# Optimization experiments

Hardware: AMD Instinct MI355X
Metric: run time of the kernel (lower is better)

The kernel has to match this reference:

```python
import jax, jax.numpy as jnp
import numpy as np
from jax import lax


def ternarize(w):
    """Standard TWN ternarization with straight-through estimator.
    delta = 0.7*mean(|w|); alpha = mean(|w|) over kept entries; w_t = alpha*sign(w)*mask.
    """
    a = jnp.abs(w)
    delta = 0.7 * a.mean()
    mask = (a > delta).astype(w.dtype)
    alpha = (a * mask).sum() / jnp.maximum(mask.sum(), 1.0)
    wt = alpha * jnp.sign(w) * mask
    return w + lax.stop_gradient(wt - w)  # STE


def conv3x3(x, w, b):
    y = lax.conv_general_dilated(x, ternarize(w), window_strides=(1, 1),
                                 padding=((1, 1), (1, 1)),
                                 dimension_numbers=('NCHW', 'OIHW', 'NCHW'))
    return y + b[None, :, None, None]


def maxpool2(x):
    return lax.reduce_window(x, -jnp.inf, lax.max, (1, 1, 2, 2), (1, 1, 2, 2), 'VALID')


def setup_inputs() -> dict:
    key = jax.random.key(0)
    ks = jax.random.split(key, 11)
    s = lambda k, shape, scale: jax.random.normal(k, shape, dtype=jnp.float32) * scale
    return {
        'x':   s(ks[0], (1024, 3, 32, 32), 1.0),
        'w1':  s(ks[1], (64, 3, 3, 3), 0.1),
        'b1':  s(ks[2], (64,), 0.01),
        'w2':  s(ks[3], (128, 64, 3, 3), 0.05),
        'b2':  s(ks[4], (128,), 0.01),
        'w3':  s(ks[5], (256, 128, 3, 3), 0.03),
        'b3':  s(ks[6], (256,), 0.01),
        'wf1': s(ks[7], (256, 4096), 0.02),
        'bf1': s(ks[8], (256,), 0.01),
        'wf2': s(ks[9], (10, 256), 0.06),
        'bf2': s(ks[10], (10,), 0.01),
    }


def reference(x, w1, b1, w2, b2, w3, b3, wf1, bf1, wf2, bf2):
    x = maxpool2(jax.nn.relu(conv3x3(x, w1, b1)))   # [B,64,16,16]
    x = maxpool2(jax.nn.relu(conv3x3(x, w2, b2)))   # [B,128,8,8]
    x = maxpool2(jax.nn.relu(conv3x3(x, w3, b3)))   # [B,256,4,4]
    x = x.reshape(-1, 256 * 4 * 4)
    x = jax.nn.relu(x @ ternarize(wf1).T + bf1)     # [B,256]
    return x @ ternarize(wf2).T + bf2               # [B,10]
```

## Files before the change

kernel.cpp:

```cpp
#include <hip/hip_runtime.h>
#include <hip/hip_bf16.h>


typedef __attribute__((ext_vector_type(8))) short short8;
typedef __attribute__((ext_vector_type(4))) float f32x4;
typedef __attribute__((ext_vector_type(4))) int i32x4;

#define GLOAD_LDS16(g, l)                                              \
    __builtin_amdgcn_global_load_lds(                                  \
        (const __attribute__((address_space(1))) void*)(g),            \
        (__attribute__((address_space(3))) void*)(l), 16, 0, 0)

__device__ __forceinline__ unsigned short f2bf(float x) {
    unsigned u = __float_as_uint(x);
    return (unsigned short)((u + 0x7fffu + ((u >> 16) & 1u)) >> 16);
}
__device__ __forceinline__ float bf2f(unsigned short b) {
    return __uint_as_float(((unsigned)b) << 16);
}

__device__ __forceinline__ float calc_S1(const double* __restrict__ scr,
                                         float amaxx) {
    const double c2 = scr[2];
    const float alpha1 = (float)(scr[1] / (c2 > 1.0 ? c2 : 1.0));
    const float ub = alpha1 * (float)scr[22] * amaxx + (float)scr[23];
    return 32512.0f / fmaxf(ub, 1e-30f);
}

#define WS_W1B   0
#define N_W1B    2048
#define WS_W2P   (WS_W1B + N_W1B)
#define N_W2P    (9*128*64)
#define WS_W3P   (WS_W2P + N_W2P)
#define N_W3P    (9*256*128)
#define WS_WTF1  (WS_W3P + N_W3P)
#define N_WTF1   (256*4096)
#define WS_WTF2  (WS_WTF1 + N_WTF1)
#define N_WTF2   (10*256)
#define WS_A1    (WS_WTF2 + N_WTF2)
#define N_A1     (1024*256*64)
#define WS_A2    (WS_A1 + N_A1)
#define N_A2     (1024*64*128)
#define WS_A3    (WS_A2 + N_A2)
#define N_A3     (1024*16*256)
#define WS_F1    (WS_A3 + N_A3)
#define N_F1     (1024*256)
#define WS_SCR   (WS_F1 + N_F1)

#define FC1_S    32

struct TernArgs {
    const float* w[6];
    int n[6];
};

__global__ void tern_stats1(TernArgs ta, double* __restrict__ scr) {
    const int wi = blockIdx.y;
    const float* __restrict__ w = ta.w[wi];
    const int n = ta.n[wi];
    __shared__ double red[4];
    const int lane = threadIdx.x & 63, wv = threadIdx.x >> 6;
    if (wi == 5) {
        float m = 0.f;
        for (int i = blockIdx.x * blockDim.x + threadIdx.x; i < n;
             i += gridDim.x * blockDim.x)
            m = fmaxf(m, fabsf(w[i]));
        #pragma unroll
        for (int off = 32; off > 0; off >>= 1)
            m = fmaxf(m, __shfl_down(m, off, 64));
        if (lane == 0) red[wv] = (double)m;
        __syncthreads();
        if (threadIdx.x == 0) {
            float mm = (float)fmax(fmax(red[0], red[1]), fmax(red[2], red[3]));
            atomicMax((int*)(scr + 20), __float_as_int(mm));
        }
        return;
    }
    double s = 0.0;
    for (int i = blockIdx.x * blockDim.x + threadIdx.x; i < n;
         i += gridDim.x * blockDim.x)
        s += (double)fabsf(w[i]);
    #pragma unroll
    for (int off = 32; off > 0; off >>= 1) s += __shfl_down(s, off, 64);
    if (lane == 0) red[wv] = s;
    __syncthreads();
    if (threadIdx.x == 0)
        atomicAdd(scr + wi * 4, red[0] + red[1] + red[2] + red[3]);
}

__global__ void tern_stats2(TernArgs ta, double* __restrict__ scr) {
    const int wi = blockIdx.y;
    const float* __restrict__ w = ta.w[wi];
    const int n = ta.n[wi];
    const float delta = (float)(0.7 * scr[wi * 4] / (double)n);
    double ms = 0.0, cnt = 0.0;
    for (int i = blockIdx.x * blockDim.x + threadIdx.x; i < n;
         i += gridDim.x * blockDim.x) {
        float a = fabsf(w[i]);
        if (a > delta) { ms += (double)a; cnt += 1.0; }
    }
    #pragma unroll
    for (int off = 32; off > 0; off >>= 1) {
        ms += __shfl_down(ms, off, 64);
        cnt += __shfl_down(cnt, off, 64);
    }
    __shared__ double redm[4], redc[4];
    const int lane = threadIdx.x & 63, wv = threadIdx.x >> 6;
    if (lane == 0) { redm[wv] = ms; redc[wv] = cnt; }
    __syncthreads();
    if (threadIdx.x == 0) {
        atomicAdd(scr + wi * 4 + 1, redm[0] + redm[1] + redm[2] + redm[3]);
        atomicAdd(scr + wi * 4 + 2, redc[0] + redc[1] + redc[2] + redc[3]);
    }
}

__global__ void nnz_pass(const float* __restrict__ w1,
                         const float* __restrict__ b1,
                         double* __restrict__ scr) {
    const float delta = (float)(0.7 * scr[0] / 1728.0);
    const int t = threadIdx.x;
    int cnt = 0;
    #pragma unroll
    for (int k = 0; k < 27; k++)
        cnt += (fabsf(w1[t * 27 + k]) > delta) ? 1 : 0;
    float bb = fabsf(b1[t]);
    #pragma unroll
    for (int off = 32; off > 0; off >>= 1) {
        cnt = max(cnt, __shfl_down(cnt, off, 64));
        bb = fmaxf(bb, __shfl_down(bb, off, 64));
    }
    if (t == 0) { scr[22] = (double)cnt; scr[23] = (double)bb; }
}

__global__ void tern_write_all(TernArgs ta, const double* __restrict__ scr,
                               signed char* __restrict__ w1b,
                               signed char* __restrict__ w2p8,
                               signed char* __restrict__ w3p8,
                               unsigned short* __restrict__ wtf1b,
                               float* __restrict__ wtf2) {
    const int wi = blockIdx.y;
    const float* __restrict__ w = ta.w[wi];
    const int n = ta.n[wi];
    const double* sc = scr + wi * 4;
    const float delta = (float)(0.7 * sc[0] / (double)n);
    const int i0 = blockIdx.x * blockDim.x + threadIdx.x;
    const int stride = gridDim.x * blockDim.x;

    if (wi == 0) {
        for (int i = i0; i < n; i += stride) {
            const int co = i / 27;
            const int kp = i % 27;
            float v = w[i];
            signed char s = (fabsf(v) > delta) ? (v > 0.0f ? 1 : -1) : 0;
            w1b[co * 64 + kp] = s;
            w1b[4096 + co * 64 + 32 + kp] = s;
        }
    } else if (wi == 4) {
        const double c = sc[2];
        const float alpha = (float)(sc[1] / (c > 1.0 ? c : 1.0));
        for (int i = i0; i < n; i += stride) {
            float v = w[i];
            wtf2[i] = (fabsf(v) > delta) ? (v > 0.0f ? alpha : -alpha) : 0.0f;
        }
    } else if (wi == 1 || wi == 2) {
        const int CIc = (wi == 1) ? 64 : 128;
        const int COc = (wi == 1) ? 128 : 256;
        signed char* dst = (wi == 1) ? w2p8 : w3p8;
        for (int i = i0; i < n; i += stride) {
            const int co = i / (CIc * 9);
            const int r = i % (CIc * 9);
            const int ci = r / 9, tap = r % 9;
            float v = w[i];
            signed char s = (fabsf(v) > delta) ? (v > 0.0f ? 1 : -1) : 0;
            dst[(tap * COc + co) * CIc + ci] = s;
        }
    } else {
        for (int i = i0; i < n; i += stride) {
            const int j = i >> 12;
            const int k = i & 4095;
            const int c = k >> 4, px = k & 15;
            float v = w[i];
            unsigned short s = (fabsf(v) > delta) ? (v > 0.0f ? 0x3f80 : 0xbf80) : 0;
            unsigned short* row = wtf1b + ((long)j << 13) + px * 512 + c;
            row[0] = s;
            row[256] = s;
        }
    }
}

__global__ __launch_bounds__(256) void conv1_i8(
        const float* __restrict__ x,
        const signed char* __restrict__ w1b,
        const float* __restrict__ bias,
        const double* __restrict__ scr,
        const int* __restrict__ amax_x,
        signed char* __restrict__ a1q) {
    constexpr int PL = 3472;
    __shared__ __align__(16) char X[2 * PL];

    const int b = blockIdx.x;
    const int tid = threadIdx.x;
    const float amx = fmaxf(__int_as_float(*amax_x), 1e-30f);
    const float S = 32512.0f / amx;
    const float S1 = calc_S1(scr, __int_as_float(*amax_x));

    for (int i = tid; i < 2 * PL / 16; i += 256)
        ((int4*)X)[i] = make_int4(0, 0, 0, 0);
    __syncthreads();

    for (int i = tid; i < 768; i += 256) {
        const float4 v = ((const float4*)(x + (long)b * 3072))[i];
        const int e = i * 4;
        const int ci = e >> 10;
        const int rem = e & 1023;
        const int h = rem >> 5, w = rem & 31;
        const int base = ci * 1156 + (h + 1) * 34 + (w + 1);
        const float f[4] = {v.x, v.y, v.z, v.w};
        #pragma unroll
        for (int j = 0; j < 4; j++) {
            const int q = __float2int_rn(f[j] * S);
            const int ql = (q << 24) >> 24;
            const int qh = (q - ql) >> 8;
            X[base + j] = (char)ql;
            X[PL + base + j] = (char)qh;
        }
    }
    __syncthreads();

    const int lane = tid & 63;
    const int wid = tid >> 6;
    const int lm = lane & 15;
    const int kg = lane >> 4;

    const int poff = (kg >= 2) ? PL : 0;
    int cst[16];
    #pragma unroll
    for (int j = 0; j < 16; j++) {
        const int kp = (kg & 1) * 16 + j;
        cst[j] = (kp < 27)
                     ? ((kp / 9) * 1156 + ((kp % 9) / 3) * 34 + (kp % 9) % 3)
                     : 0;
    }

    i32x4 BL[4], BH[4];
    #pragma unroll
    for (int nt = 0; nt < 4; nt++) {
        const int co = nt * 16 + lm;
        BL[nt] = *(const i32x4*)(w1b + (long)co * 64 + kg * 16);
        BH[nt] = *(const i32x4*)(w1b + 4096 + (long)co * 64 + kg * 16);
    }

    const double c2 = scr[2];
    const float alpha = (float)(scr[1] / (c2 > 1.0 ? c2 : 1.0));
    const float dq = alpha / S;
    signed char* yb = a1q + (long)b * 32768;

    for (int tt = 0; tt < 16; ++tt) {
        const int t = wid * 16 + tt;
        const int pp = t * 4 + (lm >> 2);
        const int sub = lm & 3;
        const int h = 2 * (pp >> 4) + (sub >> 1);
        const int w = 2 * (pp & 15) + (sub & 1);
        const int base = poff + h * 34 + w;
        unsigned d[4] = {0u, 0u, 0u, 0u};
        #pragma unroll
        for (int j = 0; j < 16; j++) {
            const unsigned byte = (unsigned char)X[base + cst[j]];
            d[j >> 2] |= byte << ((j & 3) * 8);
        }
        i32x4 Af;
        Af[0] = (int)d[0]; Af[1] = (int)d[1];
        Af[2] = (int)d[2]; Af[3] = (int)d[3];

        const int opp = t * 4 + kg;
        const int ho = opp >> 4, wo = opp & 15;
        signed char* yrow = yb + ((long)ho * 2048) + wo * 64;
        #pragma unroll
        for (int nt = 0; nt < 4; nt++) {
            i32x4 aL = 0, aH = 0;
            aL = __builtin_amdgcn_mfma_i32_16x16x64_i8(Af, BL[nt], aL, 0, 0, 0);
            aH = __builtin_amdgcn_mfma_i32_16x16x64_i8(Af, BH[nt], aH, 0, 0, 0);
            const int s0 = aH[0] * 256 + aL[0];
            const int s1 = aH[1] * 256 + aL[1];
            const int s2 = aH[2] * 256 + aL[2];
            const int s3 = aH[3] * 256 + aL[3];
            int sm = s0 > s1 ? s0 : s1;
            const int sn = s2 > s3 ? s2 : s3;
            sm = sm > sn ? sm : sn;
            const int co = nt * 16 + lm;
            const float o = fmaxf(dq * (float)sm + bias[co], 0.f);
            const int q = (int)(o * S1 + 0.5f);
            const int ql = (q << 24) >> 24;
            const int qh = (q + 128) >> 8;
            const int slot = (nt + ((wo + 1) >> 1) + 2 * (ho + 1)) & 3;
            const int off = slot * 16 + lm;
            yrow[off] = (char)ql;
            yrow[1024 + off] = (char)qh;
        }
    }
}

template <int CI, int HI, int CO, int HB, int WM, int WN, bool PREQ, int WIDX>
__global__ __launch_bounds__(256, 2) void conv_i8(
        const void* __restrict__ xin,
        const signed char* __restrict__ wp,
        const float* __restrict__ bias,
        const double* __restrict__ scr,
        const int* __restrict__ amax_in,
        int* __restrict__ amax_out,
        unsigned short* __restrict__ yout) {
    constexpr int CH8 = CI / 64;
    constexpr int NITER = 9 * CH8;
    constexpr int HR = HI / HB;
    constexpr int ROWS = HR + 2;
    constexpr int COLS = HI + 2;
    constexpr int NPIX = ROWS * COLS;
    constexpr int PSTR = NPIX * 64 + 32;
    constexpr int PO = HI / 2;
    constexpr int POR = HR / 2;
    constexpr int MT = 4, NT = 4;
    constexpr int RWB = HI * CI * 4;
    constexpr int RWQ = HI * 64 * 2;
    constexpr int RAWR = PREQ ? 1 : ((HB == 1) ? (ROWS - 2) : (ROWS - 1));
    static_assert(WM * WN == 4, "4 waves");
    static_assert(WM * 64 == HR * HI, "M covers slab pixels");
    static_assert(WN * 64 == CO, "N covers all co");
    static_assert(PREQ || RWB == 4096, "row must be 4096 B");
    static_assert(!PREQ || CH8 == 1, "PREQ path assumes CI==64");
    static_assert(HB <= 2, "row compaction assumes <=1 invalid row per end");
    static_assert((COLS & 1) == 0, "swizzle parity uses even COLS");

    __shared__ __align__(16) char X[2 * CH8 * PSTR];
    __shared__ __align__(16) char RAW[PREQ ? 16 : RAWR * RWB];
    __shared__ float redm[4];

    const int bimg = blockIdx.x / HB;
    const int hb = blockIdx.x % HB;
    const int tid = threadIdx.x;
    const int lane = tid & 63;
    const int wid = tid >> 6;

    float S;
    if (PREQ) S = calc_S1(scr, __int_as_float(*amax_in));
    else      S = 32512.0f / fmaxf(__int_as_float(*amax_in), 1e-30f);

    const int rlo = (hb == 0) ? 1 : 0;
    const int rhi = (hb == HB - 1) ? (ROWS - 1) : ROWS;

    if (PREQ) {
        for (int r = rlo; r < rhi; r++) {
            #pragma unroll
            for (int pl = 0; pl < 2; pl++) {
                if (wid == ((r * 2 + pl) & 3)) {
                    const int h = hb * HR + r - 1;
                    const char* src = (const char*)xin +
                        (long)(bimg * HI + h) * RWQ + pl * (RWQ / 2) +
                        lane * 16;
                    GLOAD_LDS16(src, &X[pl * PSTR + (r * COLS + 1) * 64]);
                }
            }
        }
        const int nfull = ((hb == 0) ? 1 : 0) + ((hb == HB - 1) ? 1 : 0);
        const int NP1 = ROWS * 2;
        const int NPZ = NP1 + nfull * (COLS - 2);
        for (int i = tid; i < NPZ * 2 * 4; i += 256) {
            const int u = i & 3;
            const int t = i >> 2;
            const int g = t % 2;
            const int e = t / 2;
            int p;
            if (e < NP1) {
                const int row = e >> 1;
                p = row * COLS + ((e & 1) ? (COLS - 1) : 0);
            } else {
                const int e2 = e - NP1;
                const int inFirst = (hb == 0) && (e2 < COLS - 2);
                const int fr = inFirst ? 0 : (ROWS - 1);
                const int cc = inFirst ? e2
                                       : (e2 - ((hb == 0) ? (COLS - 2) : 0));
                p = fr * COLS + 1 + cc;
            }
            *(int4*)&X[g * PSTR + p * 64 + u * 16] = make_int4(0, 0, 0, 0);
        }
    } else {
        for (int r = rlo; r < rhi; r++) {
            if (wid == (r & 3)) {
                const int h = hb * HR + r - 1;
                const int rl = r - rlo;
                const char* grow = (const char*)xin +
                                   ((long)(bimg * HI + h)) * RWB;
                #pragma unroll
                for (int j = 0; j < RWB / 1024; j++)
                    GLOAD_LDS16(grow + j * 1024 + lane * 16,
                                &RAW[rl * RWB + j * 1024]);
            }
        }
        constexpr int HALO = 2 * COLS + 2 * (ROWS - 2);
        for (int i = tid; i < HALO * 2 * CH8 * 4; i += 256) {
            const int u = i & 3;
            const int t = i >> 2;
            const int g = t % (2 * CH8);
            const int hp = t / (2 * CH8);
            int p;
            if (hp < COLS) p = hp;
            else if (hp < 2 * COLS) p = (ROWS - 1) * COLS + (hp - COLS);
            else {
                const int e = hp - 2 * COLS;
                p = (1 + (e >> 1)) * COLS + ((e & 1) ? (COLS - 1) : 0);
            }
            *(int4*)&X[g * PSTR + p * 64 + u * 16] = make_int4(0, 0, 0, 0);
        }
    }

    if (!PREQ) {
        __syncthreads();
        constexpr int NIT = RAWR * HI * (CI / 8);
        for (int i = tid; i < NIT; i += 256) {
            const int q8 = i % (CI / 8);
            const int t = i / (CI / 8);
            const int c = t % HI;
            const int rl = t / HI;
            const int r = rlo + rl;
            const uint4 vh =
                *(const uint4*)&RAW[rl * RWB + c * (CI * 4) + q8 * 16];
            const uint4 vl =
                *(const uint4*)&RAW[rl * RWB + c * (CI * 4) + CI * 2 +
                                    q8 * 16];
            const unsigned* hw = (const unsigned*)&vh;
            const unsigned* lw = (const unsigned*)&vl;
            float f[8];
            #pragma unroll
            for (int j = 0; j < 8; j++) {
                const unsigned hu = (j & 1) ? (hw[j >> 1] >> 16)
                                            : (hw[j >> 1] & 0xffffu);
                const unsigned lu = (j & 1) ? (lw[j >> 1] >> 16)
                                            : (lw[j >> 1] & 0xffffu);
                f[j] = __uint_as_float(hu << 16) + __uint_as_float(lu << 16);
            }
            unsigned pl0 = 0, pl1 = 0, ph0 = 0, ph1 = 0;
            #pragma unroll
            for (int j = 0; j < 8; j++) {
                const int qi = (int)(f[j] * S + 0.5f);
                const int sh = (j & 3) * 8;
                const unsigned lb = (unsigned)(qi & 255) << sh;
                const unsigned hbyte =
                    (unsigned)(((qi + 128) >> 8) & 255) << sh;
                if (j < 4) { pl0 |= lb; ph0 |= hbyte; }
                else       { pl1 |= lb; ph1 |= hbyte; }
            }
            const int p = r * COLS + c + 1;
            const int ch = q8 / 8;
            const int cc = (q8 * 8) & 63;
            const int slot = ((cc >> 4) + ((c + 1) >> 1) + 2 * r) & 3;
            const int base = p * 64 + slot * 16 + (cc & 15);
            *(uint2*)&X[ch * PSTR + base] = make_uint2(pl0, pl1);
            *(uint2*)&X[(CH8 + ch) * PSTR + base] = make_uint2(ph0, ph1);
        }
    }
    __syncthreads();

    const int wm = (WM == 1) ? 0 : (wid >> 1);
    const int wn = (WM == 1) ? wid : (wid & 1);
    const int lm = lane & 15;
    const int kg = lane >> 4;

    int pq[MT];
    #pragma unroll
    for (int mt = 0; mt < MT; mt++) {
        const int m = (wm * MT + mt) * 16 + lm;
        const int pp = m >> 2, sub = m & 3;
        const int lph = pp / PO, lpw = pp % PO;
        const int h = 2 * lph + (sub >> 1);
        const int w = 2 * lpw + (sub & 1);
        pq[mt] = ((h * COLS + w) << 6) | ((h & 1) << 3) | (w & 7);
    }
    const signed char* bp[NT];
    #pragma unroll
    for (int nt = 0; nt < NT; nt++) {
        const int co = (wn * NT + nt) * 16 + lm;
        bp[nt] = wp + (long)co * CI + kg * 16;
    }

    i32x4 accL[MT][NT], accH[MT][NT];
    #pragma unroll
    for (int mt = 0; mt < MT; mt++)
        #pragma unroll
        for (int nt = 0; nt < NT; nt++) { accL[mt][nt] = 0; accH[mt][nt] = 0; }

    i32x4 Bb[2][NT];
    #pragma unroll
    for (int nt = 0; nt < NT; nt++) Bb[0][nt] = *(const i32x4*)(bp[nt]);

    #pragma unroll 2
    for (int it = 0; it < NITER; ++it) {
        const int cur = it & 1, nxt = cur ^ 1;
        if (it + 1 < NITER) {
            const int it1 = it + 1;
            const int tap = it1 / CH8, ch1 = it1 % CH8;
            const int woff = tap * CO * CI + ch1 * 64;
            #pragma unroll
            for (int nt = 0; nt < NT; nt++)
                Bb[nxt][nt] = *(const i32x4*)(bp[nt] + woff);
        }
        const int tap = it / CH8, ch = it % CH8;
        const int ty = tap / 3, tx = tap % 3;
        const int DT = (ty * COLS + tx) << 6;
        const int typ = ty & 1;
        int ao[MT];
        #pragma unroll
        for (int mt = 0; mt < MT; mt++) {
            const int q = pq[mt];
            const int slot = (kg + ((((q >> 3) & 1) + typ) & 1) * 2 +
                              (((q & 7) + tx) >> 1)) & 3;
            ao[mt] = (q & ~63) + DT + (slot << 4);
        }
        {
            i32x4 Af[MT];
            #pragma unroll
            for (int mt = 0; mt < MT; mt++)
                Af[mt] = *(const i32x4*)&X[ch * PSTR + ao[mt]];
            #pragma unroll
            for (int mt = 0; mt < MT; mt++)
                #pragma unroll
                for (int nt = 0; nt < NT; nt++)
                    accL[mt][nt] = __builtin_amdgcn_mfma_i32_16x16x64_i8(
                        Af[mt], Bb[cur][nt], accL[mt][nt], 0, 0, 0);
        }
        {
            i32x4 Af[MT];
            #pragma unroll
            for (int mt = 0; mt < MT; mt++)
                Af[mt] = *(const i32x4*)&X[(CH8 + ch) * PSTR + ao[mt]];
            #pragma unroll
            for (int mt = 0; mt < MT; mt++)
                #pragma unroll
                for (int nt = 0; nt < NT; nt++)
                    accH[mt][nt] = __builtin_amdgcn_mfma_i32_16x16x64_i8(
                        Af[mt], Bb[cur][nt], accH[mt][nt], 0, 0, 0);
        }
    }

    const double* wst = scr + WIDX * 4;
    const double c2 = wst[2];
    const float alpha = (float)(wst[1] / (c2 > 1.0 ? c2 : 1.0));
    const float dq = alpha / S;
    float tmax = 0.f;
    #pragma unroll
    for (int mt = 0; mt < MT; mt++) {
        const int pp = (wm * MT + mt) * 4 + kg;
        const int lph = pp / PO, lpw = pp % PO;
        const int gpp = (hb * POR + lph) * PO + lpw;
        unsigned short* yr = yout + ((long)bimg * (PO * PO) + gpp) * (2 * CO);
        #pragma unroll
        for (int nt = 0; nt < NT; nt++) {
            const int co = (wn * NT + nt) * 16 + lm;
            const i32x4 aL = accL[mt][nt], aH = accH[mt][nt];
            int s0 = aH[0] * 256 + aL[0];
            int s1 = aH[1] * 256 + aL[1];
            int s2 = aH[2] * 256 + aL[2];
            int s3 = aH[3] * 256 + aL[3];
            int sm = s0 > s1 ? s0 : s1;
            int sn = s2 > s3 ? s2 : s3;
            sm = sm > sn ? sm : sn;
            float o = fmaxf(dq * (float)sm + bias[co], 0.f);
            tmax = fmaxf(tmax, o);
            unsigned short hi = f2bf(o);
            unsigned short lo = f2bf(o - bf2f(hi));
            yr[co] = hi;
            yr[CO + co] = lo;
        }
    }
    if (amax_out) {
        #pragma unroll
        for (int off = 32; off > 0; off >>= 1)
            tmax = fmaxf(tmax, __shfl_down(tmax, off, 64));
        if (lane == 0) redm[wid] = tmax;
        __syncthreads();
        if (tid == 0) {
            float m = fmaxf(fmaxf(redm[0], redm[1]), fmaxf(redm[2], redm[3]));
            atomicMax(amax_out, __float_as_int(m));
        }
    }
}

template <int S>
__global__ __launch_bounds__(256) void fc1_mfma(
        const unsigned short* __restrict__ A,
        const unsigned short* __restrict__ Bw,
        float* __restrict__ parts) {
    constexpr int KCH = 8192 / S;
    constexpr int NSTEP = KCH / 32;
    const int m0 = blockIdx.x * 128;
    const int n0 = blockIdx.y * 128;
    const int s = blockIdx.z;
    const int tid = threadIdx.x;
    const int lane = tid & 63, wid = tid >> 6;
    const int wm = wid >> 1, wn = wid & 1;
    const int lm = lane & 15, kg = lane >> 4;

    const long k0 = (long)s * KCH + kg * 8;
    const unsigned short* ap[4];
    const unsigned short* bp[4];
    #pragma unroll
    for (int t = 0; t < 4; t++) {
        ap[t] = A + (long)(m0 + wm * 64 + t * 16 + lm) * 8192 + k0;
        bp[t] = Bw + (long)(n0 + wn * 64 + t * 16 + lm) * 8192 + k0;
    }

    f32x4 acc[4][4] = {};
    short8 Ab[2][4], Bb[2][4];
    #pragma unroll
    for (int t = 0; t < 4; t++) {
        Ab[0][t] = *(const short8*)(ap[t]);
        Bb[0][t] = *(const short8*)(bp[t]);
    }

    #pragma unroll 2
    for (int st = 0; st < NSTEP; ++st) {
        const int cur = st & 1, nxt = cur ^ 1;
        if (st + 1 < NSTEP) {
            const int off = (st + 1) * 32;
            #pragma unroll
            for (int t = 0; t < 4; t++) {
                Ab[nxt][t] = *(const short8*)(ap[t] + off);
                Bb[nxt][t] = *(const short8*)(bp[t] + off);
            }
        }
        #pragma unroll
        for (int mt = 0; mt < 4; mt++)
            #pragma unroll
            for (int nt = 0; nt < 4; nt++)
                acc[mt][nt] = __builtin_amdgcn_mfma_f32_16x16x32_bf16(
                    Ab[cur][mt], Bb[cur][nt], acc[mt][nt], 0, 0, 0);
    }

    #pragma unroll
    for (int mt = 0; mt < 4; mt++) {
        #pragma unroll
        for (int r = 0; r < 4; r++) {
            const int b = m0 + wm * 64 + mt * 16 + kg * 4 + r;
            #pragma unroll
            for (int nt = 0; nt < 4; nt++) {
                const int j = n0 + wn * 64 + nt * 16 + lm;
                parts[((long)s * 1024 + b) * 256 + j] = acc[mt][nt][r];
            }
        }
    }
}

template <int S>
__global__ __launch_bounds__(256) void fc2_fused(
        const float* __restrict__ parts,
        const double* __restrict__ scr,
        const float* __restrict__ bf1v,
        const float* __restrict__ wtf2,
        const float* __restrict__ bf2v,
        float* __restrict__ out) {
    __shared__ float sf[256];
    const int b = blockIdx.x;
    const int j = threadIdx.x;
    float s = 0.f;
    #pragma unroll
    for (int p = 0; p < S; p++)
        s += parts[(long)p * 262144 + (long)b * 256 + j];
    const double c2 = scr[2];
    const float alpha = (float)(scr[1] / (c2 > 1.0 ? c2 : 1.0));
    sf[j] = fmaxf(alpha * s + bf1v[j], 0.f);
    __syncthreads();
    const int lane = threadIdx.x & 63, wid = threadIdx.x >> 6;
    for (int k = wid; k < 10; k += 4) {
        const float* wr = wtf2 + k * 256;
        float acc = 0.f;
        #pragma unroll
        for (int t = 0; t < 4; t++)
            acc += sf[lane + t * 64] * wr[lane + t * 64];
        #pragma unroll
        for (int off = 32; off > 0; off >>= 1)
            acc += __shfl_down(acc, off, 64);
        if (lane == 0) out[(long)b * 10 + k] = acc + bf2v[k];
    }
}

extern "C" void kernel_launch(void* const* d_in, const int* in_sizes, int n_in,
                              void* d_out, int out_size, void* d_ws, size_t ws_size,
                              hipStream_t stream) {
    const float* x   = (const float*)d_in[0];
    const float* w1  = (const float*)d_in[1];
    const float* b1  = (const float*)d_in[2];
    const float* w2  = (const float*)d_in[3];
    const float* b2  = (const float*)d_in[4];
    const float* w3  = (const float*)d_in[5];
    const float* b3  = (const float*)d_in[6];
    const float* wf1 = (const float*)d_in[7];
    const float* bf1 = (const float*)d_in[8];
    const float* wf2 = (const float*)d_in[9];
    const float* bf2 = (const float*)d_in[10];
    float* out = (float*)d_out;
    float* ws = (float*)d_ws;

    const int B = 1024;

    signed char*    w1b   = (signed char*)(ws + WS_W1B);
    signed char*    w2p8  = (signed char*)(ws + WS_W2P);
    signed char*    w3p8  = (signed char*)(ws + WS_W3P);
    unsigned short* wtf1b = (unsigned short*)(ws + WS_WTF1);
    float*          wtf2  = ws + WS_WTF2;
    signed char*    a1q   = (signed char*)(ws + WS_A1);
    unsigned short* a2p   = (unsigned short*)(ws + WS_A2);
    unsigned short* a3p   = (unsigned short*)(ws + WS_A3);
    double*         scr   = (double*)(ws + WS_SCR);
    int*            iscr  = (int*)(scr + 20);
    int*            amaxx = iscr;
    int*            amax2 = iscr + 2;
    float*          parts = ws + WS_A1;

    hipMemsetAsync(scr, 0, 24 * sizeof(double), stream);
    hipMemsetAsync(w1b, 0, 8192, stream);

    TernArgs ta;
    ta.w[0] = w1;  ta.n[0] = 64 * 27;
    ta.w[1] = w2;  ta.n[1] = 128 * 64 * 9;
    ta.w[2] = w3;  ta.n[2] = 256 * 128 * 9;
    ta.w[3] = wf1; ta.n[3] = 256 * 4096;
    ta.w[4] = wf2; ta.n[4] = 10 * 256;
    ta.w[5] = x;   ta.n[5] = 1024 * 3 * 32 * 32;

    hipLaunchKernelGGL(tern_stats1, dim3(128, 6), dim3(256), 0, stream, ta, scr);
    hipLaunchKernelGGL(tern_stats2, dim3(128, 5), dim3(256), 0, stream, ta, scr);
    hipLaunchKernelGGL(nnz_pass, dim3(1), dim3(64), 0, stream, w1, b1, scr);
    hipLaunchKernelGGL(tern_write_all, dim3(128, 5), dim3(256), 0, stream,
                       ta, scr, w1b, w2p8, w3p8, wtf1b, wtf2);

    hipLaunchKernelGGL(conv1_i8, dim3(B), dim3(256), 0, stream,
                       x, w1b, b1, scr, amaxx, a1q);

    hipLaunchKernelGGL((conv_i8<64, 16, 128, 2, 2, 2, true, 1>), dim3(B * 2),
                       dim3(256), 0, stream, a1q, w2p8, b2, scr, amaxx,
                       amax2, a2p);

    hipLaunchKernelGGL((conv_i8<128, 8, 256, 1, 1, 4, false, 2>), dim3(B),
                       dim3(256), 0, stream, a2p, w3p8, b3, scr, amax2,
                       (int*)nullptr, a3p);

    hipLaunchKernelGGL((fc1_mfma<FC1_S>), dim3(8, 2, FC1_S), dim3(256), 0, stream,
                       a3p, wtf1b, parts);

    hipLaunchKernelGGL((fc2_fused<FC1_S>), dim3(B), dim3(256), 0, stream,
                       parts, scr + 12, bf1, wtf2, bf2, out);
}
```

Before: 284.1 us.

## Quantize conv2 output to int8 planes using a conv1-amax bound, split conv blocks finer

Conv2 now writes its output directly as int8 hi/lo planes in the swizzled layout conv3 expects. The quantization scale comes from an a-priori bound built from conv1's amax and the nnz and bias statistics of w2, which nnz_pass now also computes. This removes conv3's bf16 unpack and requantize stage and the conv2 amax reduction. It also halves the output bytes of conv2. Both convs now use smaller per-block tiles (MT=2, more blocks, conv3 split over output channels) with launch bounds of 3 for occupancy, at the cost of reloading input per channel half and using a looser, conservative scale.

```diff
diff --git a/kernel.cpp b/kernel.cpp
--- a/kernel.cpp
+++ b/kernel.cpp
@@ -24,6 +24,13 @@
     const double c2 = scr[2];
     const float alpha1 = (float)(scr[1] / (c2 > 1.0 ? c2 : 1.0));
     const float ub = alpha1 * (float)scr[22] * amaxx + (float)scr[23];
+    return 32512.0f / fmaxf(ub, 1e-30f);
+}
+__device__ __forceinline__ float calc_S2(const double* __restrict__ scr,
+                                         float amax1) {
+    const double c2 = scr[6];
+    const float alpha2 = (float)(scr[5] / (c2 > 1.0 ? c2 : 1.0));
+    const float ub = alpha2 * (float)scr[24] * amax1 + (float)scr[25];
     return 32512.0f / fmaxf(ub, 1e-30f);
 }
 
@@ -116,20 +123,43 @@
 
 __global__ void nnz_pass(const float* __restrict__ w1,
                          const float* __restrict__ b1,
+                         const float* __restrict__ w2,
+                         const float* __restrict__ b2,
                          double* __restrict__ scr) {
-    const float delta = (float)(0.7 * scr[0] / 1728.0);
+    __shared__ int sc1[2], sc2[2];
+    __shared__ float sb1[2], sb2[2];
     const int t = threadIdx.x;
-    int cnt = 0;
-    #pragma unroll
-    for (int k = 0; k < 27; k++)
-        cnt += (fabsf(w1[t * 27 + k]) > delta) ? 1 : 0;
-    float bb = fabsf(b1[t]);
+    const int lane = t & 63, wv = t >> 6;
+
+    const float d1 = (float)(0.7 * scr[0] / 1728.0);
+    int c1 = 0; float bb1 = 0.f;
+    if (t < 64) {
+        #pragma unroll
+        for (int k = 0; k < 27; k++)
+            c1 += (fabsf(w1[t * 27 + k]) > d1) ? 1 : 0;
+        bb1 = fabsf(b1[t]);
+    }
+    const float d2 = (float)(0.7 * scr[4] / 73728.0);
+    int c2 = 0;
+    for (int k = 0; k < 576; k++)
+        c2 += (fabsf(w2[t * 576 + k]) > d2) ? 1 : 0;
+    float bb2 = fabsf(b2[t & 127]);
+
     #pragma unroll
     for (int off = 32; off > 0; off >>= 1) {
-        cnt = max(cnt, __shfl_down(cnt, off, 64));
-        bb = fmaxf(bb, __shfl_down(bb, off, 64));
-    }
-    if (t == 0) { scr[22] = (double)cnt; scr[23] = (double)bb; }
+        c1 = max(c1, __shfl_down(c1, off, 64));
+        c2 = max(c2, __shfl_down(c2, off, 64));
+        bb1 = fmaxf(bb1, __shfl_down(bb1, off, 64));
+        bb2 = fmaxf(bb2, __shfl_down(bb2, off, 64));
+    }
+    if (lane == 0) { sc1[wv] = c1; sc2[wv] = c2; sb1[wv] = bb1; sb2[wv] = bb2; }
+    __syncthreads();
+    if (t == 0) {
+        scr[22] = (double)max(sc1[0], sc1[1]);
+        scr[23] = (double)fmaxf(sb1[0], sb1[1]);
+        scr[24] = (double)max(sc2[0], sc2[1]);
+        scr[25] = (double)fmaxf(sb2[0], sb2[1]);
+    }
 }
 
 __global__ void tern_write_all(TernArgs ta, const double* __restrict__ scr,
@@ -194,9 +224,11 @@
         const float* __restrict__ bias,
         const double* __restrict__ scr,
         const int* __restrict__ amax_x,
+        int* __restrict__ amax_out,
         signed char* __restrict__ a1q) {
     constexpr int PL = 3472;
     __shared__ __align__(16) char X[2 * PL];
+    __shared__ float redm[4];
 
     const int b = blockIdx.x;
     const int tid = threadIdx.x;
@@ -253,6 +285,7 @@
     const double c2 = scr[2];
     const float alpha = (float)(scr[1] / (c2 > 1.0 ? c2 : 1.0));
     const float dq = alpha / S;
+    float tmax = 0.f;
     signed char* yb = a1q + (long)b * 32768;
 
     for (int tt = 0; tt < 16; ++tt) {
@@ -289,6 +322,7 @@
             sm = sm > sn ? sm : sn;
             const int co = nt * 16 + lm;
             const float o = fmaxf(dq * (float)sm + bias[co], 0.f);
+            tmax = fmaxf(tmax, o);
             const int q = (int)(o * S1 + 0.5f);
             const int ql = (q << 24) >> 24;
             const int qh = (q + 128) >> 8;
@@ -298,19 +332,31 @@
             yrow[1024 + off] = (char)qh;
         }
     }
-}
-
-template <int CI, int HI, int CO, int HB, int WM, int WN, bool PREQ, int WIDX>
-__global__ __launch_bounds__(256, 2) void conv_i8(
-        const void* __restrict__ xin,
+
+    #pragma unroll
+    for (int off = 32; off > 0; off >>= 1)
+        tmax = fmaxf(tmax, __shfl_down(tmax, off, 64));
+    if (lane == 0) redm[wid] = tmax;
+    __syncthreads();
+    if (tid == 0) {
+        float m = fmaxf(fmaxf(redm[0], redm[1]), fmaxf(redm[2], redm[3]));
+        atomicMax(amax_out, __float_as_int(m));
+    }
+}
+
+template <int CI, int HI, int CO, int COF, int HB, bool OUTQ, int WIDX>
+__global__ __launch_bounds__(256, 3) void conv_i8(
+        const signed char* __restrict__ xin,
         const signed char* __restrict__ wp,
         const float* __restrict__ bias,
         const double* __restrict__ scr,
-        const int* __restrict__ amax_in,
-        int* __restrict__ amax_out,
-        unsigned short* __restrict__ yout) {
+        const int* __restrict__ amax_a,
+        const int* __restrict__ amax_b,
+        void* __restrict__ yout) {
     constexpr int CH8 = CI / 64;
     constexpr int NITER = 9 * CH8;
+    constexpr int CSPL = COF / CO;
+    constexpr int NSPLIT = HB * CSPL;
     constexpr int HR = HI / HB;
     constexpr int ROWS = HR + 2;
     constexpr int COLS = HI + 2;
@@ -318,56 +364,66 @@
     constexpr int PSTR = NPIX * 64 + 32;
     constexpr int PO = HI / 2;
     constexpr int POR = HR / 2;
-    constexpr int MT = 4, NT = 4;
-    constexpr int RWB = HI * CI * 4;
-    constexpr int RWQ = HI * 64 * 2;
-    constexpr int RAWR = PREQ ? 1 : ((HB == 1) ? (ROWS - 2) : (ROWS - 1));
-    static_assert(WM * WN == 4, "4 waves");
-    static_assert(WM * 64 == HR * HI, "M covers slab pixels");
-    static_assert(WN * 64 == CO, "N covers all co");
-    static_assert(PREQ || RWB == 4096, "row must be 4096 B");
-    static_assert(!PREQ || CH8 == 1, "PREQ path assumes CI==64");
-    static_assert(HB <= 2, "row compaction assumes <=1 invalid row per end");
+    constexpr int MT = 2, NT = 4;
+    constexpr int NPL = 2 * CH8;
+    constexpr int RWQ = HI * 64 * NPL;
+    static_assert(2 * MT * 16 == HR * HI, "M coverage (WM=2)");
+    static_assert(2 * NT * 16 == CO, "N coverage (WN=2)");
+    static_assert(CI == 64 ? HI == 16 : HI == 8, "staging shape");
+    static_assert(RWQ == 2048, "row bytes");
     static_assert((COLS & 1) == 0, "swizzle parity uses even COLS");
 
-    __shared__ __align__(16) char X[2 * CH8 * PSTR];
-    __shared__ __align__(16) char RAW[PREQ ? 16 : RAWR * RWB];
-    __shared__ float redm[4];
-
-    const int bimg = blockIdx.x / HB;
-    const int hb = blockIdx.x % HB;
+    __shared__ __align__(16) char X[NPL * PSTR];
+    __shared__ __align__(16) char RAW2[(CI == 128) ? 16384 : 16];
+
+    const int bx = blockIdx.x;
+    const int bimg = bx / NSPLIT;
+    const int rem = bx % NSPLIT;
+    const int coh = (CSPL > 1) ? (rem % CSPL) : 0;
+    const int hb = (CSPL > 1) ? (rem / CSPL) : rem;
     const int tid = threadIdx.x;
     const int lane = tid & 63;
     const int wid = tid >> 6;
 
-    float S;
-    if (PREQ) S = calc_S1(scr, __int_as_float(*amax_in));
-    else      S = 32512.0f / fmaxf(__int_as_float(*amax_in), 1e-30f);
+    const float S_in = (CI == 64)
+                           ? calc_S1(scr, __int_as_float(*amax_a))
+                           : calc_S2(scr, __int_as_float(*amax_a));
 
     const int rlo = (hb == 0) ? 1 : 0;
     const int rhi = (hb == HB - 1) ? (ROWS - 1) : ROWS;
 
-    if (PREQ) {
+    if (CI == 64) {
         for (int r = rlo; r < rhi; r++) {
             #pragma unroll
             for (int pl = 0; pl < 2; pl++) {
                 if (wid == ((r * 2 + pl) & 3)) {
                     const int h = hb * HR + r - 1;
-                    const char* src = (const char*)xin +
-                        (long)(bimg * HI + h) * RWQ + pl * (RWQ / 2) +
-                        lane * 16;
+                    const signed char* src = xin +
+                        (long)(bimg * HI + h) * RWQ + pl * 1024 + lane * 16;
                     GLOAD_LDS16(src, &X[pl * PSTR + (r * COLS + 1) * 64]);
                 }
             }
         }
+    } else {
+        #pragma unroll
+        for (int j = 0; j < 16; j++) {
+            if (wid == (j & 3)) {
+                const signed char* src = xin + (long)bimg * 16384 +
+                                         j * 1024 + lane * 16;
+                GLOAD_LDS16(src, &RAW2[j * 1024]);
+            }
+        }
+    }
+
+    {
         const int nfull = ((hb == 0) ? 1 : 0) + ((hb == HB - 1) ? 1 : 0);
         const int NP1 = ROWS * 2;
         const int NPZ = NP1 + nfull * (COLS - 2);
-        for (int i = tid; i < NPZ * 2 * 4; i += 256) {
+        for (int i = tid; i < NPZ * NPL * 4; i += 256) {
             const int u = i & 3;
             const int t = i >> 2;
-            const int g = t % 2;
-            const int e = t / 2;
+            const int g = t % NPL;
+            const int e = t / NPL;
             int p;
             if (e < NP1) {
                 const int row = e >> 1;
@@ -382,85 +438,25 @@
             }
             *(int4*)&X[g * PSTR + p * 64 + u * 16] = make_int4(0, 0, 0, 0);
         }
-    } else {
-        for (int r = rlo; r < rhi; r++) {
-            if (wid == (r & 3)) {
-                const int h = hb * HR + r - 1;
-                const int rl = r - rlo;
-                const char* grow = (const char*)xin +
-                                   ((long)(bimg * HI + h)) * RWB;
-                #pragma unroll
-                for (int j = 0; j < RWB / 1024; j++)
-                    GLOAD_LDS16(grow + j * 1024 + lane * 16,
-                                &RAW[rl * RWB + j * 1024]);
-            }
-        }
-        constexpr int HALO = 2 * COLS + 2 * (ROWS - 2);
-        for (int i = tid; i < HALO * 2 * CH8 * 4; i += 256) {
-            const int u = i & 3;
-            const int t = i >> 2;
-            const int g = t % (2 * CH8);
-            const int hp = t / (2 * CH8);
-            int p;
-            if (hp < COLS) p = hp;
-            else if (hp < 2 * COLS) p = (ROWS - 1) * COLS + (hp - COLS);
-            else {
-                const int e = hp - 2 * COLS;
-                p = (1 + (e >> 1)) * COLS + ((e & 1) ? (COLS - 1) : 0);
-            }
-            *(int4*)&X[g * PSTR + p * 64 + u * 16] = make_int4(0, 0, 0, 0);
-        }
-    }
-
-    if (!PREQ) {
+    }
+
+    if (CI == 128) {
         __syncthreads();
-        constexpr int NIT = RAWR * HI * (CI / 8);
-        for (int i = tid; i < NIT; i += 256) {
-            const int q8 = i % (CI / 8);
-            const int t = i / (CI / 8);
-            const int c = t % HI;
-            const int rl = t / HI;
-            const int r = rlo + rl;
-            const uint4 vh =
-                *(const uint4*)&RAW[rl * RWB + c * (CI * 4) + q8 * 16];
-            const uint4 vl =
-                *(const uint4*)&RAW[rl * RWB + c * (CI * 4) + CI * 2 +
-                                    q8 * 16];
-            const unsigned* hw = (const unsigned*)&vh;
-            const unsigned* lw = (const unsigned*)&vl;
-            float f[8];
-            #pragma unroll
-            for (int j = 0; j < 8; j++) {
-                const unsigned hu = (j & 1) ? (hw[j >> 1] >> 16)
-                                            : (hw[j >> 1] & 0xffffu);
-                const unsigned lu = (j & 1) ? (lw[j >> 1] >> 16)
-                                            : (lw[j >> 1] & 0xffffu);
-                f[j] = __uint_as_float(hu << 16) + __uint_as_float(lu << 16);
-            }
-            unsigned pl0 = 0, pl1 = 0, ph0 = 0, ph1 = 0;
-            #pragma unroll
-            for (int j = 0; j < 8; j++) {
-                const int qi = (int)(f[j] * S + 0.5f);
-                const int sh = (j & 3) * 8;
-                const unsigned lb = (unsigned)(qi & 255) << sh;
-                const unsigned hbyte =
-                    (unsigned)(((qi + 128) >> 8) & 255) << sh;
-                if (j < 4) { pl0 |= lb; ph0 |= hbyte; }
-                else       { pl1 |= lb; ph1 |= hbyte; }
-            }
-            const int p = r * COLS + c + 1;
-            const int ch = q8 / 8;
-            const int cc = (q8 * 8) & 63;
-            const int slot = ((cc >> 4) + ((c + 1) >> 1) + 2 * r) & 3;
-            const int base = p * 64 + slot * 16 + (cc & 15);
-            *(uint2*)&X[ch * PSTR + base] = make_uint2(pl0, pl1);
-            *(uint2*)&X[(CH8 + ch) * PSTR + base] = make_uint2(ph0, ph1);
+        #pragma unroll
+        for (int k = 0; k < 4; k++) {
+            const int u = tid + k * 256;
+            const int h = u >> 7;
+            const int v = u & 127;
+            const int g = v >> 5;
+            const int b = (v & 31) << 4;
+            const int4 d = *(const int4*)&RAW2[u << 4];
+            *(int4*)&X[g * PSTR + ((h + 1) * COLS + 1) * 64 + b] = d;
         }
     }
     __syncthreads();
 
-    const int wm = (WM == 1) ? 0 : (wid >> 1);
-    const int wn = (WM == 1) ? wid : (wid & 1);
+    const int wm = wid >> 1;
+    const int wn = wid & 1;
     const int lm = lane & 15;
     const int kg = lane >> 4;
 
@@ -477,8 +473,8 @@
     const signed char* bp[NT];
     #pragma unroll
     for (int nt = 0; nt < NT; nt++) {
-        const int co = (wn * NT + nt) * 16 + lm;
-        bp[nt] = wp + (long)co * CI + kg * 16;
+        const int co_g = coh * CO + (wn * NT + nt) * 16 + lm;
+        bp[nt] = wp + (long)co_g * CI + kg * 16;
     }
 
     i32x4 accL[MT][NT], accH[MT][NT];
@@ -497,7 +493,7 @@
         if (it + 1 < NITER) {
             const int it1 = it + 1;
             const int tap = it1 / CH8, ch1 = it1 % CH8;
-            const int woff = tap * CO * CI + ch1 * 64;
+            const int woff = tap * COF * CI + ch1 * 64;
             #pragma unroll
             for (int nt = 0; nt < NT; nt++)
                 Bb[nxt][nt] = *(const i32x4*)(bp[nt] + woff);
@@ -543,42 +539,65 @@
     const double* wst = scr + WIDX * 4;
     const double c2 = wst[2];
     const float alpha = (float)(wst[1] / (c2 > 1.0 ? c2 : 1.0));
-    const float dq = alpha / S;
-    float tmax = 0.f;
-    #pragma unroll
-    for (int mt = 0; mt < MT; mt++) {
-        const int pp = (wm * MT + mt) * 4 + kg;
-        const int lph = pp / PO, lpw = pp % PO;
-        const int gpp = (hb * POR + lph) * PO + lpw;
-        unsigned short* yr = yout + ((long)bimg * (PO * PO) + gpp) * (2 * CO);
-        #pragma unroll
-        for (int nt = 0; nt < NT; nt++) {
-            const int co = (wn * NT + nt) * 16 + lm;
-            const i32x4 aL = accL[mt][nt], aH = accH[mt][nt];
-            int s0 = aH[0] * 256 + aL[0];
-            int s1 = aH[1] * 256 + aL[1];
-            int s2 = aH[2] * 256 + aL[2];
-            int s3 = aH[3] * 256 + aL[3];
-            int sm = s0 > s1 ? s0 : s1;
-            int sn = s2 > s3 ? s2 : s3;
-            sm = sm > sn ? sm : sn;
-            float o = fmaxf(dq * (float)sm + bias[co], 0.f);
-            tmax = fmaxf(tmax, o);
-            unsigned short hi = f2bf(o);
-            unsigned short lo = f2bf(o - bf2f(hi));
-            yr[co] = hi;
-            yr[CO + co] = lo;
-        }
-    }
-    if (amax_out) {
-        #pragma unroll
-        for (int off = 32; off > 0; off >>= 1)
-            tmax = fmaxf(tmax, __shfl_down(tmax, off, 64));
-        if (lane == 0) redm[wid] = tmax;
-        __syncthreads();
-        if (tid == 0) {
-            float m = fmaxf(fmaxf(redm[0], redm[1]), fmaxf(redm[2], redm[3]));
-            atomicMax(amax_out, __float_as_int(m));
+    const float dq = alpha / S_in;
+    if (OUTQ) {
+        const float S2 = calc_S2(scr, __int_as_float(*amax_b));
+        signed char* oq = (signed char*)yout;
+        #pragma unroll
+        for (int mt = 0; mt < MT; mt++) {
+            const int pp = (wm * MT + mt) * 4 + kg;
+            const int lph = pp / PO, lpw = pp % PO;
+            const int h = hb * POR + lph;
+            const int w = lpw;
+            #pragma unroll
+            for (int nt = 0; nt < NT; nt++) {
+                const int co2 = (wn * NT + nt) * 16 + lm;
+                const i32x4 aL = accL[mt][nt], aH = accH[mt][nt];
+                int s0 = aH[0] * 256 + aL[0];
+                int s1 = aH[1] * 256 + aL[1];
+                int s2 = aH[2] * 256 + aL[2];
+                int s3 = aH[3] * 256 + aL[3];
+                int sm = s0 > s1 ? s0 : s1;
+                int sn = s2 > s3 ? s2 : s3;
+                sm = sm > sn ? sm : sn;
+                const float o = fmaxf(dq * (float)sm + bias[co2], 0.f);
+                const int q = (int)(o * S2 + 0.5f);
+                const int ql = (q << 24) >> 24;
+                const int qh = (q + 128) >> 8;
+                const int slot = (((co2 >> 4) & 3) + ((w + 1) >> 1) +
+                                  2 * (h + 1)) & 3;
+                const long base = (long)bimg * 16384 + h * 2048 +
+                                  (co2 >> 6) * 512 + w * 64 + slot * 16 +
+                                  (co2 & 15);
+                oq[base] = (char)ql;
+                oq[base + 1024] = (char)qh;
+            }
+        }
+    } else {
+        unsigned short* yo = (unsigned short*)yout;
+        #pragma unroll
+        for (int mt = 0; mt < MT; mt++) {
+            const int pp = (wm * MT + mt) * 4 + kg;
+            const int lph = pp / PO, lpw = pp % PO;
+            const int gpp = (hb * POR + lph) * PO + lpw;
+            unsigned short* yr = yo + ((long)bimg * (PO * PO) + gpp) * (2 * COF);
+            #pragma unroll
+            for (int nt = 0; nt < NT; nt++) {
+                const int co_g = coh * CO + (wn * NT + nt) * 16 + lm;
+                const i32x4 aL = accL[mt][nt], aH = accH[mt][nt];
+                int s0 = aH[0] * 256 + aL[0];
+                int s1 = aH[1] * 256 + aL[1];
+                int s2 = aH[2] * 256 + aL[2];
+                int s3 = aH[3] * 256 + aL[3];
+                int sm = s0 > s1 ? s0 : s1;
+                int sn = s2 > s3 ? s2 : s3;
+                sm = sm > sn ? sm : sn;
+                float o = fmaxf(dq * (float)sm + bias[co_g], 0.f);
+                unsigned short hi = f2bf(o);
+                unsigned short lo = f2bf(o - bf2f(hi));
+                yr[co_g] = hi;
+                yr[COF + co_g] = lo;
+            }
         }
     }
 }
@@ -706,15 +725,15 @@
     unsigned short* wtf1b = (unsigned short*)(ws + WS_WTF1);
     float*          wtf2  = ws + WS_WTF2;
     signed char*    a1q   = (signed char*)(ws + WS_A1);
-    unsigned short* a2p   = (unsigned short*)(ws + WS_A2);
+    signed char*    a2q   = (signed char*)(ws + WS_A2);
     unsigned short* a3p   = (unsigned short*)(ws + WS_A3);
     double*         scr   = (double*)(ws + WS_SCR);
     int*            iscr  = (int*)(scr + 20);
     int*            amaxx = iscr;
-    int*            amax2 = iscr + 2;
+    int*            amax1 = iscr + 1;
     float*          parts = ws + WS_A1;
 
-    hipMemsetAsync(scr, 0, 24 * sizeof(double), stream);
+    hipMemsetAsync(scr, 0, 26 * sizeof(double), stream);
     hipMemsetAsync(w1b, 0, 8192, stream);
 
     TernArgs ta;
@@ -727,20 +746,21 @@
 
     hipLaunchKernelGGL(tern_stats1, dim3(128, 6), dim3(256), 0, stream, ta, scr);
     hipLaunchKernelGGL(tern_stats2, dim3(128, 5), dim3(256), 0, stream, ta, scr);
-    hipLaunchKernelGGL(nnz_pass, dim3(1), dim3(64), 0, stream, w1, b1, scr);
+    hipLaunchKernelGGL(nnz_pass, dim3(1), dim3(128), 0, stream,
+                       w1, b1, w2, b2, scr);
     hipLaunchKernelGGL(tern_write_all, dim3(128, 5), dim3(256), 0, stream,
                        ta, scr, w1b, w2p8, w3p8, wtf1b, wtf2);
 
     hipLaunchKernelGGL(conv1_i8, dim3(B), dim3(256), 0, stream,
-                       x, w1b, b1, scr, amaxx, a1q);
-
-    hipLaunchKernelGGL((conv_i8<64, 16, 128, 2, 2, 2, true, 1>), dim3(B * 2),
+                       x, w1b, b1, scr, amaxx, amax1, a1q);
+
+    hipLaunchKernelGGL((conv_i8<64, 16, 128, 128, 4, true, 1>), dim3(B * 4),
                        dim3(256), 0, stream, a1q, w2p8, b2, scr, amaxx,
-                       amax2, a2p);
-
-    hipLaunchKernelGGL((conv_i8<128, 8, 256, 1, 1, 4, false, 2>), dim3(B),
-                       dim3(256), 0, stream, a2p, w3p8, b3, scr, amax2,
-                       (int*)nullptr, a3p);
+                       amax1, a2q);
+
+    hipLaunchKernelGGL((conv_i8<128, 8, 128, 256, 1, false, 2>), dim3(B * 2),
+                       dim3(256), 0, stream, a2q, w3p8, b3, scr, amax1,
+                       amax1, a3p);
 
     hipLaunchKernelGGL((fc1_mfma<FC1_S>), dim3(8, 2, FC1_S), dim3(256), 0, stream,
                        a3p, wtf1b, parts);
```

Result: slower. 331.4 us (+16.7%).
